# Performance work log

Hardware: AMD Instinct MI355X
Metric: run time of the kernel (lower is better)

Reference implementation:

```python
import jax, jax.numpy as jnp
import numpy as np

B, T, D, DE, S, P = 16384, 2, 1024, 512, 4, 4  # batch, tasks, inp_dim, expt_dim, share, specific


def setup_inputs() -> dict:
    key = jax.random.key(0)
    ks = jax.random.split(key, 8)
    sc = 0.02
    return {
        "x0": jax.random.normal(ks[0], (B, D), jnp.float32),
        "x1": jax.random.normal(ks[1], (B, D), jnp.float32),
        "W_share": jax.random.normal(ks[2], (S, D, DE), jnp.float32) * sc,
        "b_share": jnp.zeros((S, DE), jnp.float32),
        "W_spcf": jax.random.normal(ks[3], (T, P, D, DE), jnp.float32) * sc,
        "b_spcf": jnp.zeros((T, P, DE), jnp.float32),
        "W_gate": jax.random.normal(ks[4], (T, D, S + P), jnp.float32) * sc,
        "b_gate": jnp.zeros((T, S + P), jnp.float32),
    }


def reference(x0, x1, W_share, b_share, W_spcf, b_spcf, W_gate, b_gate):
    # cat_x: [B, T, D]
    x = jnp.stack([x0, x1], axis=1)
    # per-task gate over all S+P experts: [B, T, S+P]
    gates = jax.nn.softmax(jnp.einsum("btd,tde->bte", x, W_gate) + b_gate, axis=-1)
    # shared experts applied to every task's input: [B, T, S, DE]
    share = jax.nn.relu(jnp.einsum("btd,sdf->btsf", x, W_share) + b_share[None, None])
    # task-specific experts applied to their own task input: [B, T, P, DE]
    spcf = jax.nn.relu(jnp.einsum("btd,tpdf->btpf", x, W_spcf) + b_spcf[None])
    experts = jnp.concatenate([share, spcf], axis=2)  # [B, T, S+P, DE]
    # softmax-gated mixture: [B, T, DE] (== list of per-task [B, DE] in the original)
    return jnp.einsum("bte,btef->btf", gates, experts)
```

## Files before the change

kernel.cpp:

```cpp
#include <hip/hip_runtime.h>
#include <stdint.h>

#define kB  16384
#define kD  1024
#define kDE 512

typedef __bf16 bf16x8 __attribute__((ext_vector_type(8)));
typedef float  f32x4  __attribute__((ext_vector_type(4)));

__device__ __forceinline__ unsigned short f2bf(float f) {
    union { float f; unsigned u; } v; v.f = f;
    unsigned r = v.u + 0x7FFFu + ((v.u >> 16) & 1u);
    return (unsigned short)(r >> 16);
}

__device__ __forceinline__ void async16(unsigned short* lds, const unsigned short* g) {
    __builtin_amdgcn_global_load_lds(
        (const __attribute__((address_space(1))) unsigned int*)g,
        (__attribute__((address_space(3))) unsigned int*)lds, 16, 0, 0);
}

__global__ __launch_bounds__(256) void prep_w(const float* __restrict__ Wsh,
                                              const float* __restrict__ Wsp,
                                              unsigned short* __restrict__ Wt) {
    __shared__ float tile[32][33];
    const int slot = blockIdx.z;
    const int k0 = blockIdx.x * 32;
    const int n0 = blockIdx.y * 32;
    const float* src = (slot < 4) ? (Wsh + (size_t)slot * kD * kDE)
                                  : (Wsp + (size_t)(slot - 4) * kD * kDE);
    const int tx = threadIdx.x, ty = threadIdx.y;
#pragma unroll
    for (int i = 0; i < 4; i++)
        tile[ty + i * 8][tx] = src[(size_t)(k0 + ty + i * 8) * kDE + n0 + tx];
    __syncthreads();
    unsigned short* dst = Wt + (size_t)slot * kDE * kD;
#pragma unroll
    for (int i = 0; i < 4; i++)
        dst[(size_t)(n0 + ty + i * 8) * kD + k0 + tx] = f2bf(tile[tx][ty + i * 8]);
}

__global__ __launch_bounds__(256) void prep_b(const float* __restrict__ bsh,
                                              const float* __restrict__ bsp,
                                              float* __restrict__ bc) {
    int i = blockIdx.x * 256 + threadIdx.x;
    int n = i & 511, e = (i >> 9) & 7, t = i >> 12;
    bc[i] = (e < 4) ? bsh[e * 512 + n] : bsp[(t * 4 + (e - 4)) * 512 + n];
}

__global__ __launch_bounds__(256) void conv_gate(
    const float* __restrict__ x0, const float* __restrict__ x1,
    const float* __restrict__ Wg, const float* __restrict__ bg,
    unsigned short* __restrict__ xb, float* __restrict__ g) {
    const int wid = threadIdx.x >> 6, lane = threadIdx.x & 63;
    const int r = blockIdx.x * 4 + wid;
    const int t = r >> 14, b = r & 16383;
    const float* xrow = (t ? x1 : x0) + (size_t)b * kD;
    unsigned short* xbrow = xb + (size_t)(t * kB + b) * kD;
    const float* Wgt = Wg + t * kD * 8;
    float p[8] = {0.f,0.f,0.f,0.f,0.f,0.f,0.f,0.f};
#pragma unroll
    for (int it = 0; it < 4; it++) {
        const int d0 = it * 256 + lane * 4;
        const float4 v = *(const float4*)(xrow + d0);
        ushort4 h;
        h.x = f2bf(v.x); h.y = f2bf(v.y); h.z = f2bf(v.z); h.w = f2bf(v.w);
        *(ushort4*)(xbrow + d0) = h;
        const float xv[4] = {v.x, v.y, v.z, v.w};
#pragma unroll
        for (int j = 0; j < 4; j++) {
            const float* wrow = Wgt + (size_t)(d0 + j) * 8;
#pragma unroll
            for (int e = 0; e < 8; e++) p[e] += xv[j] * wrow[e];
        }
    }
#pragma unroll
    for (int e = 0; e < 8; e++) {
        float v = p[e];
#pragma unroll
        for (int s = 1; s < 64; s <<= 1) v += __shfl_xor(v, s, 64);
        p[e] = v;
    }
    float lg[8];
#pragma unroll
    for (int e = 0; e < 8; e++) lg[e] = p[e] + bg[t * 8 + e];
    float mx = lg[0];
#pragma unroll
    for (int e = 1; e < 8; e++) mx = fmaxf(mx, lg[e]);
    float s = 0.f;
#pragma unroll
    for (int e = 0; e < 8; e++) { lg[e] = __expf(lg[e] - mx); s += lg[e]; }
    const float inv = 1.f / s;
    if (lane == 0) {
        float* gp = g + (size_t)(t * kB + b) * 8;
        float4 g0 = {lg[0]*inv, lg[1]*inv, lg[2]*inv, lg[3]*inv};
        float4 g1 = {lg[4]*inv, lg[5]*inv, lg[6]*inv, lg[7]*inv};
        *(float4*)gp = g0;
        *(float4*)(gp + 4) = g1;
    }
}

__global__ __launch_bounds__(256, 2) void moe_gemm(
    const unsigned short* __restrict__ xb, const unsigned short* __restrict__ Wt,
    const float* __restrict__ g, const float* __restrict__ bc,
    float* __restrict__ out) {
    __shared__ __align__(16) unsigned short As[128 * 64];
    __shared__ __align__(16) unsigned short Bs[128 * 64];
    const int rt = blockIdx.x, ct = blockIdx.y, t = blockIdx.z;
    const int tid = threadIdx.x, wid = tid >> 6, lane = tid & 63;
    const int wr = wid >> 1, wc = wid & 1;
    const int rowBase = rt * 128, n0 = ct * 128;

    const int srow = wid * 32 + (lane >> 3);
    const int swzk = (((lane & 7) ^ ((lane >> 3) & 7)) << 3);
    const unsigned short* aG0 = xb + (size_t)t * kB * kD +
                                (size_t)(rowBase + srow) * kD + swzk;
    unsigned short* aL = As + wid * 2048;
    unsigned short* bL = Bs + wid * 2048;

    const int rA = wr * 64 + (lane & 15);
    const int rB = wc * 64 + (lane & 15);
    const int c0 = (((lane >> 4) ^ (lane & 7)) << 3);

    f32x4 oacc[4][4];
#pragma unroll
    for (int m = 0; m < 4; m++)
#pragma unroll
        for (int n = 0; n < 4; n++) oacc[m][n] = (f32x4){0.f, 0.f, 0.f, 0.f};

    for (int e = 0; e < 8; e++) {
        const int slot = (e < 4) ? e : (4 + t * 4 + (e - 4));
        const unsigned short* bG0 = Wt + (size_t)slot * kDE * kD +
                                    (size_t)(n0 + srow) * kD + swzk;
        f32x4 acc[4][4];
#pragma unroll
        for (int m = 0; m < 4; m++)
#pragma unroll
            for (int n = 0; n < 4; n++) acc[m][n] = (f32x4){0.f, 0.f, 0.f, 0.f};

        for (int kt = 0; kt < 16; kt++) {
            const int k0 = kt * 64;
            __syncthreads();
#pragma unroll
            for (int i = 0; i < 4; i++) async16(aL + i * 512, aG0 + k0 + i * 8192);
#pragma unroll
            for (int i = 0; i < 4; i++) async16(bL + i * 512, bG0 + k0 + i * 8192);
            __syncthreads();
#pragma unroll
            for (int ks = 0; ks < 2; ks++) {
                const int cs = c0 ^ (ks << 5);
                bf16x8 af[4], bfr[4];
#pragma unroll
                for (int m = 0; m < 4; m++)
                    af[m] = *(const bf16x8*)&As[(rA + m * 16) * 64 + cs];
#pragma unroll
                for (int n = 0; n < 4; n++)
                    bfr[n] = *(const bf16x8*)&Bs[(rB + n * 16) * 64 + cs];
#pragma unroll
                for (int m = 0; m < 4; m++)
#pragma unroll
                    for (int n = 0; n < 4; n++)
                        acc[m][n] = __builtin_amdgcn_mfma_f32_16x16x32_bf16(
                            af[m], bfr[n], acc[m][n], 0, 0, 0);
            }
        }
        const float* gE  = g  + (size_t)t * kB * 8 + e;
        const float* bcE = bc + (t * 8 + e) * kDE + n0 + wc * 64;
        float bv[4];
#pragma unroll
        for (int n = 0; n < 4; n++) bv[n] = bcE[n * 16 + (lane & 15)];
#pragma unroll
        for (int m = 0; m < 4; m++) {
            const int r0 = rowBase + wr * 64 + m * 16 + ((lane >> 4) << 2);
            float gv[4];
#pragma unroll
            for (int q = 0; q < 4; q++) gv[q] = gE[(size_t)(r0 + q) * 8];
#pragma unroll
            for (int n = 0; n < 4; n++)
#pragma unroll
                for (int q = 0; q < 4; q++)
                    oacc[m][n][q] += gv[q] * fmaxf(acc[m][n][q] + bv[n], 0.f);
        }
    }
#pragma unroll
    for (int m = 0; m < 4; m++) {
        const int r0 = rowBase + wr * 64 + m * 16 + ((lane >> 4) << 2);
#pragma unroll
        for (int n = 0; n < 4; n++) {
            const int col = n0 + wc * 64 + n * 16 + (lane & 15);
#pragma unroll
            for (int q = 0; q < 4; q++)
                out[((size_t)(r0 + q) * 2 + t) * kDE + col] = oacc[m][n][q];
        }
    }
}

extern "C" void kernel_launch(void* const* d_in, const int* in_sizes, int n_in,
                              void* d_out, int out_size, void* d_ws, size_t ws_size,
                              hipStream_t stream) {
    const float* x0  = (const float*)d_in[0];
    const float* x1  = (const float*)d_in[1];
    const float* Wsh = (const float*)d_in[2];
    const float* bsh = (const float*)d_in[3];
    const float* Wsp = (const float*)d_in[4];
    const float* bsp = (const float*)d_in[5];
    const float* Wg  = (const float*)d_in[6];
    const float* bg  = (const float*)d_in[7];
    float* out = (float*)d_out;

    char* ws = (char*)d_ws;
    unsigned short* xb = (unsigned short*)ws;
    unsigned short* Wt = (unsigned short*)(ws + 67108864);
    float* g  = (float*)(ws + 67108864 + 12582912);
    float* bc = (float*)(ws + 67108864 + 12582912 + 1048576);

    prep_w<<<dim3(32, 16, 12), dim3(32, 8), 0, stream>>>(Wsh, Wsp, Wt);
    prep_b<<<dim3(32), dim3(256), 0, stream>>>(bsh, bsp, bc);
    conv_gate<<<dim3(8192), dim3(256), 0, stream>>>(x0, x1, Wg, bg, xb, g);
    moe_gemm<<<dim3(128, 4, 2), dim3(256), 0, stream>>>(xb, Wt, g, bc, out);
}
```

Measured before the change: 428.6 us.

## Restructure MoE GEMM to compute all 8 experts per tile with double-buffered LDS

The GEMM kernel now uses 512-thread blocks that hold accumulators for all 8 experts of a 128x64 output tile at once. The A tile is loaded from global memory once per k-step and reused across all experts, instead of being reloaded for each expert. LDS is double-buffered with asynchronous loads and explicit vmcnt waits so the next tile's loads overlap the current tile's MFMAs. Block indices are remapped to group tiles for cache locality. In exchange, the per-block LDS footprint (about 160 KB) and the accumulator register count go up, which can limit occupancy.

```diff
diff --git a/kernel.cpp b/kernel.cpp
--- a/kernel.cpp
+++ b/kernel.cpp
@@ -100,99 +100,111 @@
     }
 }
 
-__global__ __launch_bounds__(256, 2) void moe_gemm(
+__global__ __launch_bounds__(512, 2) void moe_gemm(
     const unsigned short* __restrict__ xb, const unsigned short* __restrict__ Wt,
     const float* __restrict__ g, const float* __restrict__ bc,
     float* __restrict__ out) {
-    __shared__ __align__(16) unsigned short As[128 * 64];
-    __shared__ __align__(16) unsigned short Bs[128 * 64];
-    const int rt = blockIdx.x, ct = blockIdx.y, t = blockIdx.z;
+    __shared__ __align__(16) unsigned short As[2][128 * 64];
+    __shared__ __align__(16) unsigned short Bs[2][8 * 64 * 64];
+
+    const int bid = blockIdx.x;
+    const int swz = (bid & 7) * 256 + (bid >> 3);
+    const int ct = swz & 7;
+    const int rt = (swz >> 3) & 127;
+    const int t  = swz >> 10;
+    const int n0 = ct * 64;
+
     const int tid = threadIdx.x, wid = tid >> 6, lane = tid & 63;
-    const int wr = wid >> 1, wc = wid & 1;
-    const int rowBase = rt * 128, n0 = ct * 128;
-
-    const int srow = wid * 32 + (lane >> 3);
-    const int swzk = (((lane & 7) ^ ((lane >> 3) & 7)) << 3);
-    const unsigned short* aG0 = xb + (size_t)t * kB * kD +
-                                (size_t)(rowBase + srow) * kD + swzk;
-    unsigned short* aL = As + wid * 2048;
-    unsigned short* bL = Bs + wid * 2048;
-
-    const int rA = wr * 64 + (lane & 15);
-    const int rB = wc * 64 + (lane & 15);
-    const int c0 = (((lane >> 4) ^ (lane & 7)) << 3);
-
-    f32x4 oacc[4][4];
-#pragma unroll
-    for (int m = 0; m < 4; m++)
-#pragma unroll
-        for (int n = 0; n < 4; n++) oacc[m][n] = (f32x4){0.f, 0.f, 0.f, 0.f};
-
-    for (int e = 0; e < 8; e++) {
-        const int slot = (e < 4) ? e : (4 + t * 4 + (e - 4));
-        const unsigned short* bG0 = Wt + (size_t)slot * kDE * kD +
-                                    (size_t)(n0 + srow) * kD + swzk;
-        f32x4 acc[4][4];
-#pragma unroll
-        for (int m = 0; m < 4; m++)
-#pragma unroll
-            for (int n = 0; n < 4; n++) acc[m][n] = (f32x4){0.f, 0.f, 0.f, 0.f};
-
-        for (int kt = 0; kt < 16; kt++) {
-            const int k0 = kt * 64;
-            __syncthreads();
-#pragma unroll
-            for (int i = 0; i < 4; i++) async16(aL + i * 512, aG0 + k0 + i * 8192);
-#pragma unroll
-            for (int i = 0; i < 4; i++) async16(bL + i * 512, bG0 + k0 + i * 8192);
-            __syncthreads();
-#pragma unroll
-            for (int ks = 0; ks < 2; ks++) {
-                const int cs = c0 ^ (ks << 5);
-                bf16x8 af[4], bfr[4];
-#pragma unroll
-                for (int m = 0; m < 4; m++)
-                    af[m] = *(const bf16x8*)&As[(rA + m * 16) * 64 + cs];
-#pragma unroll
-                for (int n = 0; n < 4; n++)
-                    bfr[n] = *(const bf16x8*)&Bs[(rB + n * 16) * 64 + cs];
-#pragma unroll
-                for (int m = 0; m < 4; m++)
-#pragma unroll
-                    for (int n = 0; n < 4; n++)
-                        acc[m][n] = __builtin_amdgcn_mfma_f32_16x16x32_bf16(
-                            af[m], bfr[n], acc[m][n], 0, 0, 0);
-            }
+    const int wr = wid >> 2, wc = wid & 3;
+
+    const int swzChunk = ((lane & 7) ^ ((lane >> 3) & 7)) * 8;
+    const unsigned short* aSrc = xb + (size_t)t * kB * kD +
+        (size_t)(rt * 128 + wid * 16 + (lane >> 3)) * kD + swzChunk;
+    const int slot = (wid < 4) ? wid : (4 + t * 4 + (wid - 4));
+    const unsigned short* bSrc = Wt + (size_t)slot * kDE * kD +
+        (size_t)(n0 + (lane >> 3)) * kD + swzChunk;
+
+    const int rAbase = (wr * 64 + (lane & 15)) * 64;
+    const int bOff   = (wc * 16 + (lane & 15)) * 64;
+    const int lx     = lane & 7;
+    const int kg     = lane >> 4;
+
+    f32x4 acc[8][4];
+#pragma unroll
+    for (int e = 0; e < 8; e++)
+#pragma unroll
+        for (int m = 0; m < 4; m++) acc[e][m] = (f32x4){0.f, 0.f, 0.f, 0.f};
+
+#define STAGE(buf, kt)                                                        \
+    {                                                                         \
+        const int k0_ = (kt) * 64;                                            \
+        _Pragma("unroll")                                                     \
+        for (int i = 0; i < 2; i++)                                           \
+            async16(&As[buf][wid * 1024 + i * 512], aSrc + k0_ + i * 8 * kD); \
+        _Pragma("unroll")                                                     \
+        for (int j = 0; j < 8; j++)                                           \
+            async16(&Bs[buf][wid * 4096 + j * 512], bSrc + k0_ + j * 8 * kD); \
+    }
+
+#define COMPUTE(buf)                                                          \
+    {                                                                         \
+        _Pragma("unroll")                                                     \
+        for (int ks = 0; ks < 2; ks++) {                                      \
+            const int p8 = ((ks * 4 + kg) ^ lx) * 8;                          \
+            bf16x8 af[4];                                                     \
+            _Pragma("unroll")                                                 \
+            for (int m = 0; m < 4; m++)                                       \
+                af[m] = *(const bf16x8*)&As[buf][rAbase + m * 1024 + p8];     \
+            _Pragma("unroll")                                                 \
+            for (int e = 0; e < 8; e++) {                                     \
+                bf16x8 bf = *(const bf16x8*)&Bs[buf][e * 4096 + bOff + p8];   \
+                _Pragma("unroll")                                             \
+                for (int m = 0; m < 4; m++)                                   \
+                    acc[e][m] = __builtin_amdgcn_mfma_f32_16x16x32_bf16(      \
+                        af[m], bf, acc[e][m], 0, 0, 0);                       \
+            }                                                                 \
+        }                                                                     \
+    }
+
+    STAGE(0, 0);
+    for (int kt = 0; kt < 15; ++kt) {
+        STAGE((kt + 1) & 1, kt + 1);
+        asm volatile("s_waitcnt vmcnt(10)" ::: "memory");
+        __builtin_amdgcn_s_barrier();
+        COMPUTE(kt & 1);
+        __builtin_amdgcn_s_barrier();
+    }
+    asm volatile("s_waitcnt vmcnt(0)" ::: "memory");
+    __builtin_amdgcn_s_barrier();
+    COMPUTE(1);
+
+    const int col = n0 + wc * 16 + (lane & 15);
+    float bv[8];
+#pragma unroll
+    for (int e = 0; e < 8; e++) bv[e] = bc[(t * 8 + e) * kDE + col];
+
+#pragma unroll
+    for (int m = 0; m < 4; m++) {
+        const int r0 = rt * 128 + wr * 64 + m * 16 + kg * 4;
+        f32x4 oq = (f32x4){0.f, 0.f, 0.f, 0.f};
+#pragma unroll
+        for (int q = 0; q < 4; q++) {
+            const float* gp = g + ((size_t)t * kB + r0 + q) * 8;
+            const float4 ga = *(const float4*)gp;
+            const float4 gb = *(const float4*)(gp + 4);
+            const float gv[8] = {ga.x, ga.y, ga.z, ga.w, gb.x, gb.y, gb.z, gb.w};
+            float s = 0.f;
+#pragma unroll
+            for (int e = 0; e < 8; e++)
+                s += gv[e] * fmaxf(acc[e][m][q] + bv[e], 0.f);
+            oq[q] = s;
         }
-        const float* gE  = g  + (size_t)t * kB * 8 + e;
-        const float* bcE = bc + (t * 8 + e) * kDE + n0 + wc * 64;
-        float bv[4];
-#pragma unroll
-        for (int n = 0; n < 4; n++) bv[n] = bcE[n * 16 + (lane & 15)];
-#pragma unroll
-        for (int m = 0; m < 4; m++) {
-            const int r0 = rowBase + wr * 64 + m * 16 + ((lane >> 4) << 2);
-            float gv[4];
-#pragma unroll
-            for (int q = 0; q < 4; q++) gv[q] = gE[(size_t)(r0 + q) * 8];
-#pragma unroll
-            for (int n = 0; n < 4; n++)
-#pragma unroll
-                for (int q = 0; q < 4; q++)
-                    oacc[m][n][q] += gv[q] * fmaxf(acc[m][n][q] + bv[n], 0.f);
-        }
-    }
-#pragma unroll
-    for (int m = 0; m < 4; m++) {
-        const int r0 = rowBase + wr * 64 + m * 16 + ((lane >> 4) << 2);
-#pragma unroll
-        for (int n = 0; n < 4; n++) {
-            const int col = n0 + wc * 64 + n * 16 + (lane & 15);
-#pragma unroll
-            for (int q = 0; q < 4; q++)
-                out[((size_t)(r0 + q) * 2 + t) * kDE + col] = oacc[m][n][q];
-        }
-    }
+#pragma unroll
+        for (int q = 0; q < 4; q++)
+            out[((size_t)(r0 + q) * 2 + t) * kDE + col] = oq[q];
+    }
+#undef STAGE
+#undef COMPUTE
 }
 
 extern "C" void kernel_launch(void* const* d_in, const int* in_sizes, int n_in,
@@ -217,5 +229,5 @@
     prep_w<<<dim3(32, 16, 12), dim3(32, 8), 0, stream>>>(Wsh, Wsp, Wt);
     prep_b<<<dim3(32), dim3(256), 0, stream>>>(bsh, bsp, bc);
     conv_gate<<<dim3(8192), dim3(256), 0, stream>>>(x0, x1, Wg, bg, xb, g);
-    moe_gemm<<<dim3(128, 4, 2), dim3(256), 0, stream>>>(xb, Wt, g, bc, out);
-}
+    moe_gemm<<<dim3(2048), dim3(512), 0, stream>>>(xb, Wt, g, bc, out);
+}
```

Result: faster. 415.7 us (-3.0%).
